# Performance work log

Measured on AMD Instinct MI355X. Metric: run time of the kernel, lower is better.

## Reference

```python
import jax, jax.numpy as jnp
import numpy as np

N_NODES = 100000
N_EDGES = 1600000
D_FEAT = 128
UNITS = 128
LEAKY_ALPHA = 0.2  # tf.nn.leaky_relu default


def setup_inputs() -> dict:
    key = jax.random.key(0)
    k1, k2, k3, k4 = jax.random.split(key, 4)
    node_states = jax.random.normal(k1, (N_NODES, D_FEAT), dtype=jnp.float32)
    edges = jax.random.randint(k2, (N_EDGES, 2), 0, N_NODES, dtype=jnp.int64)
    kernel = jax.random.normal(k3, (D_FEAT, UNITS), dtype=jnp.float32) * (1.0 / np.sqrt(D_FEAT))
    kernel_attention = jax.random.normal(k4, (2 * UNITS, 1), dtype=jnp.float32) * (1.0 / np.sqrt(2 * UNITS))
    return {
        "node_states": node_states,
        "edges": edges,
        "kernel": kernel,
        "kernel_attention": kernel_attention,
    }


def reference(node_states, edges, kernel, kernel_attention):
    n = node_states.shape[0]
    tgt_idx = edges[:, 0]
    src_idx = edges[:, 1]

    # node_states_transformed: [N, units]
    h = node_states @ kernel

    # Attention logits. concat([tgt, src]) @ ka == tgt @ ka_t + src @ ka_s
    # (avoids materializing the [E, 2*units] concat).
    ka_t = kernel_attention[:UNITS, 0]   # [units]
    ka_s = kernel_attention[UNITS:, 0]   # [units]
    score_t = h @ ka_t                   # [N]
    score_s = h @ ka_s                   # [N]
    e = score_t[tgt_idx] + score_s[src_idx]              # [E]
    e = jax.nn.leaky_relu(e, negative_slope=LEAKY_ALPHA)
    e = jnp.exp(jnp.clip(e, -2.0, 2.0))

    # Segment softmax over incoming edges of each target node.
    sum_e = jax.ops.segment_sum(e, tgt_idx, num_segments=n)  # [N]
    attention = e / (sum_e[tgt_idx] + 1e-9)                  # [E]

    # Weighted scatter-sum of source messages.
    messages = h[src_idx] * attention[:, None]               # [E, units]
    output = jax.ops.segment_sum(messages, tgt_idx, num_segments=n)  # [N, units]
    return output
```

## Files before the change

### kernel.cpp

```cpp
#include <hip/hip_runtime.h>
#include <stdint.h>

typedef unsigned short ushort_t;
typedef __attribute__((ext_vector_type(8))) short short8;
typedef __attribute__((ext_vector_type(4))) float float4v;
typedef __attribute__((ext_vector_type(2))) float float2v;

#define N_NODES 100000
#define N_EDGES 1600000
#define D 128
#define NB_GEMM 1563
#define NWIN    250
#define EPB     6400
#define BUCKETS 782
#define CAP     2560

static __device__ __forceinline__ float2v up2(uint32_t u) {
    float2v r;
    r.x = __builtin_bit_cast(float, u << 16);
    r.y = __builtin_bit_cast(float, u & 0xffff0000u);
    return r;
}
static __device__ __forceinline__ uint32_t f2bf_u(float f) {
    uint32_t u = __builtin_bit_cast(uint32_t, f);
    return (u + 0x7fffu + ((u >> 16) & 1u)) >> 16;
}
static __device__ __forceinline__ ushort_t f2bf(float f) {
    return (ushort_t)f2bf_u(f);
}
static __device__ __forceinline__ uint32_t pack2(float a, float b) {
    return f2bf_u(a) | (f2bf_u(b) << 16);
}
static __device__ __forceinline__ float edge_e(float s) {
    float x = (s >= 0.0f) ? s : 0.2f * s;
    x = fminf(fmaxf(x, -2.0f), 2.0f);
    return __expf(x);
}

__global__ void __launch_bounds__(256) fused_kernel(const float* __restrict__ X,
                                                    const float* __restrict__ W,
                                                    const float* __restrict__ KA,
                                                    ushort_t* __restrict__ H,
                                                    float* __restrict__ st,
                                                    float* __restrict__ ss,
                                                    int M,
                                                    const int* __restrict__ E,
                                                    int* __restrict__ sortedE,
                                                    ushort_t* __restrict__ bmat,
                                                    ushort_t* __restrict__ lofs) {
    __shared__ __align__(16) ushort_t lds_raw[16384];
    __shared__ float lds_wa[256];
    __shared__ int   ldet;
    int tid = threadIdx.x;
    if (blockIdx.x >= NB_GEMM) {
        int eb = blockIdx.x - NB_GEMM;
        int* lhist = (int*)lds_raw;
        int* lpart = ((int*)lds_raw) + 1024;
        int t = tid;
        if (t == 0) ldet = 0;
        for (int j = t; j < 1024; j += 256) lhist[j] = 0;
        __syncthreads();
        int nz = 0;
#pragma unroll
        for (int j = 0; j < 8; j++)
            if (E[(t + j * 256) * 2 + 1] != 0) nz = 1;
        if (nz) atomicOr(&ldet, 1);
        __syncthreads();
        int i64 = (ldet == 0) ? 1 : 0;
        int base = eb * EPB;
        int bin[25], w[25];
#pragma unroll
        for (int j = 0; j < 25; j++) {
            int i = base + j * 256 + t;
            int tgt, src;
            if (i64) { uint4 v = *(const uint4*)(E + (size_t)i * 4); tgt = (int)v.x; src = (int)v.z; }
            else     { uint2 v = *(const uint2*)(E + (size_t)i * 2); tgt = (int)v.x; src = (int)v.y; }
            if ((unsigned)tgt >= (unsigned)N_NODES) tgt = 0;
            if ((unsigned)src >= (unsigned)N_NODES) src = 0;
            bin[j] = tgt >> 7;
            w[j]   = ((tgt & 127) << 17) | src;
            atomicAdd(&lhist[bin[j]], 1);
        }
        __syncthreads();
        int c0 = lhist[t * 4], c1 = lhist[t * 4 + 1];
        int c2 = lhist[t * 4 + 2], c3 = lhist[t * 4 + 3];
        int sum = c0 + c1 + c2 + c3;
        lpart[t] = sum;
        __syncthreads();
        for (int off = 1; off < 256; off <<= 1) {
            int x = (t >= off) ? lpart[t - off] : 0;
            __syncthreads();
            lpart[t] += x;
            __syncthreads();
        }
        int e0 = lpart[t] - sum;
        int e1 = e0 + c0, e2 = e1 + c1, e3 = e2 + c2;
        int cc[4] = {c0, c1, c2, c3};
        int ee[4] = {e0, e1, e2, e3};
#pragma unroll
        for (int k = 0; k < 4; k++) {
            int bb = t * 4 + k;
            if (bb < BUCKETS) {
                bmat[eb * BUCKETS + bb] = (ushort_t)cc[k];
                lofs[eb * BUCKETS + bb] = (ushort_t)ee[k];
            }
        }
        lhist[t * 4] = e0; lhist[t * 4 + 1] = e1;
        lhist[t * 4 + 2] = e2; lhist[t * 4 + 3] = e3;
        __syncthreads();
#pragma unroll
        for (int j = 0; j < 25; j++) {
            int pos = atomicAdd(&lhist[bin[j]], 1);
            if (pos < EPB) sortedE[base + pos] = w[j];
        }
        return;
    }
    {
        for (int c = tid; c < 2048; c += 256) {
            int l = c & 15, q = (c >> 4) & 3, tt = (c >> 6) & 7, kb = c >> 9;
            int n = tt * 16 + l;
            int k0 = kb * 32 + q * 8;
            short8 v;
#pragma unroll
            for (int jj = 0; jj < 8; jj++)
                v[jj] = (short)f2bf(W[(size_t)(k0 + jj) * 128 + n]);
            *(short8*)(&lds_raw[((kb * 8 + tt) * 64 + q * 16 + l) * 8]) = v;
        }
        int half = tid >> 7, k = tid & 127;
        const float4* kav4  = (const float4*)(KA + half * 128);
        const float4* wrow4 = (const float4*)(W + (size_t)k * 128);
        float acc = 0.0f;
#pragma unroll 8
        for (int j = 0; j < 32; j++) {
            float4 a4 = wrow4[j], b4 = kav4[j];
            acc += a4.x * b4.x + a4.y * b4.y + a4.z * b4.z + a4.w * b4.w;
        }
        lds_wa[half * 128 + k] = acc;
    }
    __syncthreads();

    int wave = tid >> 6, lane = tid & 63;
    int quad = lane >> 4, l16 = lane & 15;
    int m0 = blockIdx.x * 64 + wave * 16;

    float4 f[8];
    {
        int ar = m0 + l16; if (ar >= M) ar = M - 1;
        const float* xr = X + (size_t)ar * D + quad * 8;
#pragma unroll
        for (int kb = 0; kb < 4; kb++) {
            f[kb * 2]     = *(const float4*)(xr + kb * 32);
            f[kb * 2 + 1] = *(const float4*)(xr + kb * 32 + 4);
        }
    }
    short8 a[4];
    float sct = 0.0f, scs = 0.0f;
#pragma unroll
    for (int kb = 0; kb < 4; kb++) {
        float4 f0 = f[kb * 2], f1 = f[kb * 2 + 1];
        const float* wt0 = lds_wa + kb * 32 + quad * 8;
        float4 t0v = *(const float4*)(wt0);
        float4 t1v = *(const float4*)(wt0 + 4);
        float4 s0v = *(const float4*)(wt0 + 128);
        float4 s1v = *(const float4*)(wt0 + 132);
        sct += f0.x * t0v.x + f0.y * t0v.y + f0.z * t0v.z + f0.w * t0v.w
             + f1.x * t1v.x + f1.y * t1v.y + f1.z * t1v.z + f1.w * t1v.w;
        scs += f0.x * s0v.x + f0.y * s0v.y + f0.z * s0v.z + f0.w * s0v.w
             + f1.x * s1v.x + f1.y * s1v.y + f1.z * s1v.z + f1.w * s1v.w;
        short8 v;
        v[0] = (short)f2bf(f0.x); v[1] = (short)f2bf(f0.y);
        v[2] = (short)f2bf(f0.z); v[3] = (short)f2bf(f0.w);
        v[4] = (short)f2bf(f1.x); v[5] = (short)f2bf(f1.y);
        v[6] = (short)f2bf(f1.z); v[7] = (short)f2bf(f1.w);
        a[kb] = v;
    }
    sct += __shfl_xor(sct, 16); sct += __shfl_xor(sct, 32);
    scs += __shfl_xor(scs, 16); scs += __shfl_xor(scs, 32);
    if (quad == 0 && m0 + l16 < M) { st[m0 + l16] = sct; ss[m0 + l16] = scs; }

    float4v acc[8] = {};
#pragma unroll
    for (int kb = 0; kb < 4; kb++) {
#pragma unroll
        for (int t = 0; t < 8; t++) {
            short8 b = *(const short8*)(&lds_raw[((kb * 8 + t) * 64 + lane) * 8]);
            acc[t] = __builtin_amdgcn_mfma_f32_16x16x32_bf16(a[kb], b, acc[t], 0, 0, 0);
        }
    }
#pragma unroll
    for (int r = 0; r < 4; r++) {
        int orow = m0 + quad * 4 + r;
        if (orow < M) {
            uint4 v;
            v.x = pack2(acc[0][r], acc[1][r]);
            v.y = pack2(acc[2][r], acc[3][r]);
            v.z = pack2(acc[4][r], acc[5][r]);
            v.w = pack2(acc[6][r], acc[7][r]);
            *(uint4*)(H + (size_t)orow * D + l16 * 8) = v;
        }
    }
}

__global__ void __launch_bounds__(512) agg2_kernel(const ushort_t* __restrict__ bmat,
                                                   const ushort_t* __restrict__ lofs,
                                                   const int* __restrict__ sortedE,
                                                   const float* __restrict__ st,
                                                   const float* __restrict__ ss,
                                                   const ushort_t* __restrict__ H,
                                                   float* __restrict__ out) {
    __shared__ int stage[CAP];
    __shared__ int sortedLoc[CAP];
    __shared__ int lh[128];
    __shared__ int lrp[129];
    __shared__ int wsum[8];
    __shared__ int lsoff[NWIN];
    __shared__ int lsst[NWIN];
    int b = blockIdx.x, t = threadIdx.x;
    int lane = t & 63, wv = t >> 6;
    int cnt = 0, sst = 0;
    if (t < NWIN) {
        cnt = bmat[t * BUCKETS + b];
        sst = lofs[t * BUCKETS + b];
    }
    int x = cnt;
#pragma unroll
    for (int off = 1; off < 64; off <<= 1) {
        int y = __shfl_up(x, off);
        if (lane >= off) x += y;
    }
    if (lane == 63) wsum[wv] = x;
    if (t < 128) lh[t] = 0;
    __syncthreads();
    int wbase = 0, total = 0;
#pragma unroll
    for (int w = 0; w < 8; w++) {
        int sv = wsum[w];
        if (w < wv) wbase += sv;
        total += sv;
    }
    if (total > CAP) total = CAP;
    int soff = wbase + x - cnt;
    if (t < NWIN) { lsoff[t] = soff; lsst[t] = sst; }
    __syncthreads();
    for (int j = t; j < total; j += 512) {
        int lo = 0, hi = NWIN - 1;
        while (lo < hi) {
            int mid = (lo + hi + 1) >> 1;
            if (lsoff[mid] <= j) lo = mid; else hi = mid - 1;
        }
        stage[j] = sortedE[lo * EPB + lsst[lo] + (j - lsoff[lo])];
    }
    __syncthreads();
    for (int j = t; j < total; j += 512)
        atomicAdd(&lh[stage[j] >> 17], 1);
    __syncthreads();
    int v = (t < 128) ? lh[t] : 0;
    int xs = v;
#pragma unroll
    for (int off = 1; off < 64; off <<= 1) {
        int y = __shfl_up(xs, off);
        if (lane >= off) xs += y;
    }
    if (t == 63) wsum[0] = xs;
    __syncthreads();
    if (t < 128) {
        int inc = (wv == 1) ? xs + wsum[0] : xs;
        int ex = inc - v;
        lrp[t] = ex;
        lh[t]  = ex;
    }
    if (t == 0) lrp[128] = total;
    __syncthreads();
    for (int j = t; j < total; j += 512) {
        int p = stage[j];
        int pos = atomicAdd(&lh[p >> 17], 1);
        if (pos < total) sortedLoc[pos] = p & 0x1FFFF;
    }
    __syncthreads();
    int g = lane >> 4, l = lane & 15;
    for (int nd = wv; nd < 128; nd += 8) {
        int gnode = b * 128 + nd;
        if (gnode >= N_NODES) break;
        int start = lrp[nd], end = lrp[nd + 1];
        float stn = st[gnode];
        float den = 0.0f;
        float2v acc2[4] = {};
        int m = start + g;
        for (; m + 12 < end; m += 16) {
            int s0 = sortedLoc[m],     s1 = sortedLoc[m + 4];
            int s2 = sortedLoc[m + 8], s3 = sortedLoc[m + 12];
            float e0 = edge_e(stn + ss[s0]);
            float e1 = edge_e(stn + ss[s1]);
            float e2 = edge_e(stn + ss[s2]);
            float e3 = edge_e(stn + ss[s3]);
            den += (e0 + e1) + (e2 + e3);
            uint4 p0 = *(const uint4*)(H + ((unsigned)s0 << 7) + l * 8);
            uint4 p1 = *(const uint4*)(H + ((unsigned)s1 << 7) + l * 8);
            uint4 p2 = *(const uint4*)(H + ((unsigned)s2 << 7) + l * 8);
            uint4 p3 = *(const uint4*)(H + ((unsigned)s3 << 7) + l * 8);
            float2v E0 = {e0, e0}, E1 = {e1, e1}, E2 = {e2, e2}, E3 = {e3, e3};
            acc2[0] += E0 * up2(p0.x) + E1 * up2(p1.x) + E2 * up2(p2.x) + E3 * up2(p3.x);
            acc2[1] += E0 * up2(p0.y) + E1 * up2(p1.y) + E2 * up2(p2.y) + E3 * up2(p3.y);
            acc2[2] += E0 * up2(p0.z) + E1 * up2(p1.z) + E2 * up2(p2.z) + E3 * up2(p3.z);
            acc2[3] += E0 * up2(p0.w) + E1 * up2(p1.w) + E2 * up2(p2.w) + E3 * up2(p3.w);
        }
        for (; m + 4 < end; m += 8) {
            int s0 = sortedLoc[m], s1 = sortedLoc[m + 4];
            float e0 = edge_e(stn + ss[s0]);
            float e1 = edge_e(stn + ss[s1]);
            den += e0 + e1;
            uint4 p0 = *(const uint4*)(H + ((unsigned)s0 << 7) + l * 8);
            uint4 p1 = *(const uint4*)(H + ((unsigned)s1 << 7) + l * 8);
            float2v E0 = {e0, e0}, E1 = {e1, e1};
            acc2[0] += E0 * up2(p0.x) + E1 * up2(p1.x);
            acc2[1] += E0 * up2(p0.y) + E1 * up2(p1.y);
            acc2[2] += E0 * up2(p0.z) + E1 * up2(p1.z);
            acc2[3] += E0 * up2(p0.w) + E1 * up2(p1.w);
        }
        if (m < end) {
            int s0 = sortedLoc[m];
            float e0 = edge_e(stn + ss[s0]);
            den += e0;
            uint4 p0 = *(const uint4*)(H + ((unsigned)s0 << 7) + l * 8);
            float2v E0 = {e0, e0};
            acc2[0] += E0 * up2(p0.x);
            acc2[1] += E0 * up2(p0.y);
            acc2[2] += E0 * up2(p0.z);
            acc2[3] += E0 * up2(p0.w);
        }
        den += __shfl_xor(den, 16);
        den += __shfl_xor(den, 32);
        float r[8];
#pragma unroll
        for (int j = 0; j < 4; j++) {
            float a0 = acc2[j].x, a1 = acc2[j].y;
            a0 += __shfl_xor(a0, 16); a0 += __shfl_xor(a0, 32);
            a1 += __shfl_xor(a1, 16); a1 += __shfl_xor(a1, 32);
            r[j * 2] = a0; r[j * 2 + 1] = a1;
        }
        float inv = 1.0f / (den + 1e-9f);
        if (g == 0) {
#pragma unroll
            for (int k = 0; k < 8; k++)
                out[(size_t)gnode * D + k * 16 + l] = r[k] * inv;
        }
    }
}

extern "C" void kernel_launch(void* const* d_in, const int* in_sizes, int n_in,
                              void* d_out, int out_size, void* d_ws, size_t ws_size,
                              hipStream_t stream) {
    const float* X  = (const float*)d_in[0];
    const int*   E  = (const int*)d_in[1];
    const float* W  = (const float*)d_in[2];
    const float* KA = (const float*)d_in[3];
    for (int i = 0; i < n_in; i++) {
        int s = in_sizes[i];
        if (s == N_NODES * D)      X  = (const float*)d_in[i];
        else if (s == N_EDGES * 2) E  = (const int*)d_in[i];
        else if (s == D * D)       W  = (const float*)d_in[i];
        else if (s == 2 * D)       KA = (const float*)d_in[i];
    }
    float* out = (float*)d_out;

    char* ws = (char*)d_ws;
    ushort_t* H        = (ushort_t*)(ws + 0);
    float*    st       = (float*)   (ws + 25601024);
    float*    ssb      = (float*)   (ws + 26001024);
    int*      sortedE  = (int*)     (ws + 26401024);
    ushort_t* bmat     = (ushort_t*)(ws + 32801024);
    ushort_t* lofs     = (ushort_t*)(ws + 33192032);

    fused_kernel<<<NB_GEMM + NWIN, 256, 0, stream>>>(X, W, KA, H, st, ssb,
                                                     N_NODES, E,
                                                     sortedE, bmat, lofs);
    agg2_kernel<<<BUCKETS, 512, 0, stream>>>(bmat, lofs, sortedE, st, ssb,
                                             H, out);
}
```

Measured before the change: 227.2 us.

## Make GEMM blocks persistent over three row tiles with X prefetch

Reduces GEMM block count threefold so each block processes three 64-row tiles, reusing the LDS-staged bf16 weight tile and the W·KA projection computed once per block. Prefetches the next tile's X rows into registers while the current tile's MFMAs run. This cuts redundant per-block weight staging, at the cost of fewer blocks (less parallelism) and higher register pressure.

```diff
diff --git a/kernel.cpp b/kernel.cpp
--- a/kernel.cpp
+++ b/kernel.cpp
@@ -10,6 +10,7 @@
 #define N_EDGES 1600000
 #define D 128
 #define NB_GEMM 1563
+#define NBG     521
 #define NWIN    250
 #define EPB     6400
 #define BUCKETS 782
@@ -52,8 +53,8 @@
     __shared__ float lds_wa[256];
     __shared__ int   ldet;
     int tid = threadIdx.x;
-    if (blockIdx.x >= NB_GEMM) {
-        int eb = blockIdx.x - NB_GEMM;
+    if (blockIdx.x >= NBG) {
+        int eb = blockIdx.x - NBG;
         int* lhist = (int*)lds_raw;
         int* lpart = ((int*)lds_raw) + 1024;
         int t = tid;
@@ -141,11 +142,11 @@
 
     int wave = tid >> 6, lane = tid & 63;
     int quad = lane >> 4, l16 = lane & 15;
-    int m0 = blockIdx.x * 64 + wave * 16;
+    int t0 = blockIdx.x;
 
     float4 f[8];
     {
-        int ar = m0 + l16; if (ar >= M) ar = M - 1;
+        int ar = t0 * 64 + wave * 16 + l16; if (ar >= M) ar = M - 1;
         const float* xr = X + (size_t)ar * D + quad * 8;
 #pragma unroll
         for (int kb = 0; kb < 4; kb++) {
@@ -153,50 +154,69 @@
             f[kb * 2 + 1] = *(const float4*)(xr + kb * 32 + 4);
         }
     }
-    short8 a[4];
-    float sct = 0.0f, scs = 0.0f;
-#pragma unroll
-    for (int kb = 0; kb < 4; kb++) {
-        float4 f0 = f[kb * 2], f1 = f[kb * 2 + 1];
-        const float* wt0 = lds_wa + kb * 32 + quad * 8;
-        float4 t0v = *(const float4*)(wt0);
-        float4 t1v = *(const float4*)(wt0 + 4);
-        float4 s0v = *(const float4*)(wt0 + 128);
-        float4 s1v = *(const float4*)(wt0 + 132);
-        sct += f0.x * t0v.x + f0.y * t0v.y + f0.z * t0v.z + f0.w * t0v.w
-             + f1.x * t1v.x + f1.y * t1v.y + f1.z * t1v.z + f1.w * t1v.w;
-        scs += f0.x * s0v.x + f0.y * s0v.y + f0.z * s0v.z + f0.w * s0v.w
-             + f1.x * s1v.x + f1.y * s1v.y + f1.z * s1v.z + f1.w * s1v.w;
-        short8 v;
-        v[0] = (short)f2bf(f0.x); v[1] = (short)f2bf(f0.y);
-        v[2] = (short)f2bf(f0.z); v[3] = (short)f2bf(f0.w);
-        v[4] = (short)f2bf(f1.x); v[5] = (short)f2bf(f1.y);
-        v[6] = (short)f2bf(f1.z); v[7] = (short)f2bf(f1.w);
-        a[kb] = v;
-    }
-    sct += __shfl_xor(sct, 16); sct += __shfl_xor(sct, 32);
-    scs += __shfl_xor(scs, 16); scs += __shfl_xor(scs, 32);
-    if (quad == 0 && m0 + l16 < M) { st[m0 + l16] = sct; ss[m0 + l16] = scs; }
-
-    float4v acc[8] = {};
-#pragma unroll
-    for (int kb = 0; kb < 4; kb++) {
-#pragma unroll
-        for (int t = 0; t < 8; t++) {
-            short8 b = *(const short8*)(&lds_raw[((kb * 8 + t) * 64 + lane) * 8]);
-            acc[t] = __builtin_amdgcn_mfma_f32_16x16x32_bf16(a[kb], b, acc[t], 0, 0, 0);
-        }
-    }
-#pragma unroll
-    for (int r = 0; r < 4; r++) {
-        int orow = m0 + quad * 4 + r;
-        if (orow < M) {
-            uint4 v;
-            v.x = pack2(acc[0][r], acc[1][r]);
-            v.y = pack2(acc[2][r], acc[3][r]);
-            v.z = pack2(acc[4][r], acc[5][r]);
-            v.w = pack2(acc[6][r], acc[7][r]);
-            *(uint4*)(H + (size_t)orow * D + l16 * 8) = v;
+#pragma unroll
+    for (int it = 0; it < 3; it++) {
+        int m0 = (t0 + it * NBG) * 64 + wave * 16;
+        float4 nf[8];
+        if (it < 2) {
+            int ar = (t0 + (it + 1) * NBG) * 64 + wave * 16 + l16;
+            if (ar >= M) ar = M - 1;
+            const float* xr = X + (size_t)ar * D + quad * 8;
+#pragma unroll
+            for (int kb = 0; kb < 4; kb++) {
+                nf[kb * 2]     = *(const float4*)(xr + kb * 32);
+                nf[kb * 2 + 1] = *(const float4*)(xr + kb * 32 + 4);
+            }
+        }
+        short8 a[4];
+        float sct = 0.0f, scs = 0.0f;
+#pragma unroll
+        for (int kb = 0; kb < 4; kb++) {
+            float4 f0 = f[kb * 2], f1 = f[kb * 2 + 1];
+            const float* wt0 = lds_wa + kb * 32 + quad * 8;
+            float4 t0v = *(const float4*)(wt0);
+            float4 t1v = *(const float4*)(wt0 + 4);
+            float4 s0v = *(const float4*)(wt0 + 128);
+            float4 s1v = *(const float4*)(wt0 + 132);
+            sct += f0.x * t0v.x + f0.y * t0v.y + f0.z * t0v.z + f0.w * t0v.w
+                 + f1.x * t1v.x + f1.y * t1v.y + f1.z * t1v.z + f1.w * t1v.w;
+            scs += f0.x * s0v.x + f0.y * s0v.y + f0.z * s0v.z + f0.w * s0v.w
+                 + f1.x * s1v.x + f1.y * s1v.y + f1.z * s1v.z + f1.w * s1v.w;
+            short8 v;
+            v[0] = (short)f2bf(f0.x); v[1] = (short)f2bf(f0.y);
+            v[2] = (short)f2bf(f0.z); v[3] = (short)f2bf(f0.w);
+            v[4] = (short)f2bf(f1.x); v[5] = (short)f2bf(f1.y);
+            v[6] = (short)f2bf(f1.z); v[7] = (short)f2bf(f1.w);
+            a[kb] = v;
+        }
+        sct += __shfl_xor(sct, 16); sct += __shfl_xor(sct, 32);
+        scs += __shfl_xor(scs, 16); scs += __shfl_xor(scs, 32);
+        if (quad == 0 && m0 + l16 < M) { st[m0 + l16] = sct; ss[m0 + l16] = scs; }
+
+        float4v acc[8] = {};
+#pragma unroll
+        for (int kb = 0; kb < 4; kb++) {
+#pragma unroll
+            for (int t = 0; t < 8; t++) {
+                short8 b = *(const short8*)(&lds_raw[((kb * 8 + t) * 64 + lane) * 8]);
+                acc[t] = __builtin_amdgcn_mfma_f32_16x16x32_bf16(a[kb], b, acc[t], 0, 0, 0);
+            }
+        }
+#pragma unroll
+        for (int r = 0; r < 4; r++) {
+            int orow = m0 + quad * 4 + r;
+            if (orow < M) {
+                uint4 v;
+                v.x = pack2(acc[0][r], acc[1][r]);
+                v.y = pack2(acc[2][r], acc[3][r]);
+                v.z = pack2(acc[4][r], acc[5][r]);
+                v.w = pack2(acc[6][r], acc[7][r]);
+                *(uint4*)(H + (size_t)orow * D + l16 * 8) = v;
+            }
+        }
+        if (it < 2) {
+#pragma unroll
+            for (int j = 0; j < 8; j++) f[j] = nf[j];
         }
     }
 }
@@ -371,9 +391,9 @@
     ushort_t* bmat     = (ushort_t*)(ws + 32801024);
     ushort_t* lofs     = (ushort_t*)(ws + 33192032);
 
-    fused_kernel<<<NB_GEMM + NWIN, 256, 0, stream>>>(X, W, KA, H, st, ssb,
-                                                     N_NODES, E,
-                                                     sortedE, bmat, lofs);
+    fused_kernel<<<NBG + NWIN, 256, 0, stream>>>(X, W, KA, H, st, ssb,
+                                                 N_NODES, E,
+                                                 sortedE, bmat, lofs);
     agg2_kernel<<<BUCKETS, 512, 0, stream>>>(bmat, lofs, sortedE, st, ssb,
                                              H, out);
 }
```

Result: faster. 208.6 us (-8.2%).
